# Kernel tuning notes

Hardware: AMD Instinct MI355X
Metric: run time of the kernel (lower is better)

The kernel has to match this reference:

```python
import jax, jax.numpy as jnp
import numpy as np

NUM_HEAD = 8
B, NO, LQ, LC, D = 16, 512, 512, 512, 1024


def setup_inputs() -> dict:
    key = jax.random.key(0)
    ks = jax.random.split(key, 32)
    s = 0.02

    def lin(i, din, dout):
        w = jax.random.normal(ks[i], (din, dout), jnp.float32) * s
        b = jax.random.normal(ks[i + 1], (dout,), jnp.float32) * s
        return w, b

    v = jax.random.normal(ks[20], (B, NO, D), jnp.float32)
    q = jax.random.normal(ks[21], (B, LQ, D), jnp.float32)
    c = jax.random.normal(ks[22], (B, LC, D), jnp.float32)
    # binary float masks; force first position valid so mask.sum > 0
    v_mask = jax.random.randint(ks[23], (B, NO), 0, 2).astype(jnp.float32).at[:, 0].set(1.0)
    q_mask = jax.random.randint(ks[24], (B, LQ), 0, 2).astype(jnp.float32).at[:, 0].set(1.0)
    c_mask = jax.random.randint(ks[25], (B, LC), 0, 2).astype(jnp.float32).at[:, 0].set(1.0)
    v4q_w, v4q_b = lin(0, D, D)
    q4v_w, q4v_b = lin(2, D, D)
    v_lin_w, v_lin_b = lin(4, D, 3 * D)
    q_lin_w, q_lin_b = lin(6, D, 3 * D)
    c_lin_w, c_lin_b = lin(8, D, 3 * D)
    v_out_w, v_out_b = lin(10, D, D)
    q_out_w, q_out_b = lin(12, D, D)
    c_out_w, c_out_b = lin(14, D, D)
    m_v_k = jax.random.normal(ks[16], (1, 1, D), jnp.float32) * s
    m_v_v = jax.random.normal(ks[17], (1, 1, D), jnp.float32) * s
    m_c_k = jax.random.normal(ks[18], (1, 1, D), jnp.float32) * s
    m_c_v = jax.random.normal(ks[19], (1, 1, D), jnp.float32) * s
    return dict(v=v, q=q, c=c, v_mask=v_mask, q_mask=q_mask, c_mask=c_mask,
                v4q_w=v4q_w, v4q_b=v4q_b, q4v_w=q4v_w, q4v_b=q4v_b,
                v_lin_w=v_lin_w, v_lin_b=v_lin_b, q_lin_w=q_lin_w, q_lin_b=q_lin_b,
                c_lin_w=c_lin_w, c_lin_b=c_lin_b,
                m_v_k=m_v_k, m_v_v=m_v_v, m_c_k=m_c_k, m_c_v=m_c_v,
                v_out_w=v_out_w, v_out_b=v_out_b, q_out_w=q_out_w, q_out_b=q_out_b,
                c_out_w=c_out_w, c_out_b=c_out_b)


def _attn(q_in, k_in, v_in, kmask):
    # q_in [B,Sq,D], k_in/v_in [B,Sk,D], kmask [B,Sk]. Vectorized over heads
    # (replaces the per-head Python loop + cat in the torch source).
    Bs, Sq, Dm = q_in.shape
    Sk = k_in.shape[1]
    dh = Dm // NUM_HEAD
    qh = q_in.reshape(Bs, Sq, NUM_HEAD, dh)
    kh = k_in.reshape(Bs, Sk, NUM_HEAD, dh)
    vh = v_in.reshape(Bs, Sk, NUM_HEAD, dh)
    scores = jnp.einsum('bqhd,bkhd->bhqk', qh, kh)
    # torch: masked_fill(-1e9) then divide by sqrt(d_head) -> replicate exactly
    scores = jnp.where(kmask[:, None, None, :] == 0, jnp.float32(-1e9), scores) / (dh ** 0.5)
    w = jax.nn.softmax(scores, axis=-1)
    out = jnp.einsum('bhqk,bkhd->bqhd', w, vh)
    return out.reshape(Bs, Sq, Dm)


def _forward(v, q, c, v_mask, q_mask, c_mask,
             v4q_w, v4q_b, q4v_w, q4v_b,
             v_lin_w, v_lin_b, q_lin_w, q_lin_b, c_lin_w, c_lin_b,
             m_v_k, m_v_v, m_c_k, m_c_v,
             v_out_w, v_out_b, q_out_w, q_out_b, c_out_w, c_out_b):
    Bs = v.shape[0]
    Dm = v_out_w.shape[0]
    relu, sig = jax.nn.relu, jax.nn.sigmoid
    v_mean = (v * v_mask[:, :, None]).sum(1) / v_mask.sum(1, keepdims=True)
    q_mean = (q * q_mask[:, :, None]).sum(1) / q_mask.sum(1, keepdims=True)
    v4q_gate = sig(relu(v_mean) @ v4q_w + v4q_b)[:, None, :]  # gates q's q/k
    q4v_gate = sig(relu(q_mean) @ q4v_w + q4v_b)[:, None, :]  # gates v's q/k
    v_trans = (relu(v) @ v_lin_w + v_lin_b) * v_mask[:, :, None]
    q_trans = (relu(q) @ q_lin_w + q_lin_b) * q_mask[:, :, None]
    c_trans = (relu(c) @ c_lin_w + c_lin_b) * c_mask[:, :, None]
    v_k, v_q, v_v = jnp.split(v_trans, 3, axis=2)
    q_k, q_q, q_v = jnp.split(q_trans, 3, axis=2)
    c_k, c_q, c_v = jnp.split(c_trans, 3, axis=2)
    # memory tokens: k scaled by sqrt(D), v scaled by sqrt(mv)=1 (as in torch)
    mvk = (Dm ** 0.5) * jnp.broadcast_to(m_v_k, (Bs, 1, Dm))
    mvv = jnp.broadcast_to(m_v_v, (Bs, 1, Dm))
    v_k = jnp.concatenate([mvk, v_k], axis=1)
    v_v = jnp.concatenate([mvv, v_v], axis=1)
    v_kmask = jnp.concatenate([jnp.ones((Bs, 1), v_mask.dtype), v_mask], axis=1)
    mck = (Dm ** 0.5) * jnp.broadcast_to(m_c_k, (Bs, 1, Dm))
    mcv = jnp.broadcast_to(m_c_v, (Bs, 1, Dm))
    c_k = jnp.concatenate([mck, c_k], axis=1)
    c_v = jnp.concatenate([mcv, c_v], axis=1)
    c_kmask = jnp.concatenate([jnp.ones((Bs, 1), c_mask.dtype), c_mask], axis=1)
    new_vq = (1.0 + q4v_gate) * v_q
    new_vk = (1.0 + q4v_gate) * v_k
    new_qq = (1.0 + v4q_gate) * q_q
    new_qk = (1.0 + v4q_gate) * q_k
    v_update = _attn(new_vq, new_vk, v_v, v_kmask)
    q_update = _attn(new_qq, new_qk, q_v, q_mask)
    c_update = _attn(c_q, c_k, c_v, c_kmask)
    updated_v = (v + v_update) @ v_out_w + v_out_b
    updated_q = (q + q_update) @ q_out_w + q_out_b
    updated_c = (c + c_update) @ c_out_w + c_out_b
    return updated_v, updated_q, updated_c


def reference(v, q, c, v_mask, q_mask, c_mask,
              v4q_w, v4q_b, q4v_w, q4v_b,
              v_lin_w, v_lin_b, q_lin_w, q_lin_b, c_lin_w, c_lin_b,
              m_v_k, m_v_v, m_c_k, m_c_v,
              v_out_w, v_out_b, q_out_w, q_out_b, c_out_w, c_out_b):
    return _forward(v, q, c, v_mask, q_mask, c_mask,
                    v4q_w, v4q_b, q4v_w, q4v_b,
                    v_lin_w, v_lin_b, q_lin_w, q_lin_b, c_lin_w, c_lin_b,
                    m_v_k, m_v_v, m_c_k, m_c_v,
                    v_out_w, v_out_b, q_out_w, q_out_b, c_out_w, c_out_b)
```

## Files before the change

### kernel.cpp

```cpp
#include <hip/hip_runtime.h>
#include <stdint.h>

typedef __attribute__((ext_vector_type(8))) short s16x8;
typedef __attribute__((ext_vector_type(4))) float f32x4;

#define DM 1024
#define TOK 512
#define LDK 3072

static __device__ __forceinline__ float bf2f(short u) {
  union { unsigned int i; float f; } x;
  x.i = ((unsigned int)(unsigned short)u) << 16;
  return x.f;
}
static __device__ __forceinline__ short f2bf(float f) {
  union { float f; unsigned int i; } x; x.f = f;
  unsigned int r = x.i + 0x7FFFu + ((x.i >> 16) & 1u);
  return (short)(r >> 16);
}
static __device__ __forceinline__ f32x4 fzero4() {
  f32x4 z; z[0]=0.f; z[1]=0.f; z[2]=0.f; z[3]=0.f; return z;
}
static __device__ __forceinline__ s16x8 szero8() {
  s16x8 z; z[0]=0; z[1]=0; z[2]=0; z[3]=0; z[4]=0; z[5]=0; z[6]=0; z[7]=0; return z;
}
static __device__ __forceinline__ void gl_lds16(const short* g, short* s) {
  __builtin_amdgcn_global_load_lds((const __attribute__((address_space(1))) void*)g,
                                   (__attribute__((address_space(3))) void*)s, 16, 0, 0);
}

#define MFMA(a, b, c) __builtin_amdgcn_mfma_f32_16x16x32_bf16(a, b, c, 0, 0, 0)

struct CastArgs { const float* x[3]; short* xb[3]; };
__global__ __launch_bounds__(256) void cast_relu_kernel(CastArgs a) {
  const float* x = a.x[blockIdx.y];
  short* xb = a.xb[blockIdx.y];
  size_t i = ((size_t)blockIdx.x * 256 + threadIdx.x) * 8;
  float4 v0 = *(const float4*)(x + i);
  float4 v1 = *(const float4*)(x + i + 4);
  s16x8 o;
  o[0] = f2bf(fmaxf(v0.x, 0.f)); o[1] = f2bf(fmaxf(v0.y, 0.f));
  o[2] = f2bf(fmaxf(v0.z, 0.f)); o[3] = f2bf(fmaxf(v0.w, 0.f));
  o[4] = f2bf(fmaxf(v1.x, 0.f)); o[5] = f2bf(fmaxf(v1.y, 0.f));
  o[6] = f2bf(fmaxf(v1.z, 0.f)); o[7] = f2bf(fmaxf(v1.w, 0.f));
  *(s16x8*)(xb + i) = o;
}

__global__ __launch_bounds__(256) void mean_kernel(const float* __restrict__ v,
                                                   const float* __restrict__ q,
                                                   const float* __restrict__ vmask,
                                                   const float* __restrict__ qmask,
                                                   float* __restrict__ vmean,
                                                   float* __restrict__ qmean) {
  int d = blockIdx.x * 256 + threadIdx.x;
  int b = blockIdx.y;
  const float* x; const float* mk; float* out;
  if (blockIdx.z == 0) { x = v; mk = vmask; out = vmean; }
  else                 { x = q; mk = qmask; out = qmean; }
  const float* xp = x + ((size_t)b * TOK) * DM + d;
  const float* mp = mk + b * TOK;
  float s = 0.f, ms = 0.f;
#pragma unroll 4
  for (int r = 0; r < TOK; ++r) {
    float m = mp[r];
    ms += m;
    s += xp[(size_t)r * DM] * m;
  }
  out[b * DM + d] = s / ms;
}

struct TransArgs { const float* w[3]; short* wt[3]; };
__global__ void transpose_cast_kernel(TransArgs a, int K, int N) {
  __shared__ float tile[32][33];
  const float* w = a.w[blockIdx.z];
  short* wt = a.wt[blockIdx.z];
  int n0 = blockIdx.x * 32, k0 = blockIdx.y * 32;
  int tx = threadIdx.x, ty = threadIdx.y;
#pragma unroll
  for (int i = 0; i < 32; i += 8)
    tile[ty + i][tx] = w[(size_t)(k0 + ty + i) * N + n0 + tx];
  __syncthreads();
#pragma unroll
  for (int i = 0; i < 32; i += 8)
    wt[(size_t)(n0 + ty + i) * K + k0 + tx] = f2bf(tile[tx][ty + i]);
}

__global__ __launch_bounds__(256) void gate_kernel(const float* __restrict__ vmean,
                                                   const float* __restrict__ qmean,
                                                   const float* __restrict__ v4q_w,
                                                   const float* __restrict__ v4q_b,
                                                   const float* __restrict__ q4v_w,
                                                   const float* __restrict__ q4v_b,
                                                   float* __restrict__ gate_q,
                                                   float* __restrict__ gate_v) {
  int n = blockIdx.x * 256 + threadIdx.x;
  int b = blockIdx.y;
  const float* mean; const float* w; const float* bias; float* out;
  if (blockIdx.z == 0) { mean = vmean; w = v4q_w; bias = v4q_b; out = gate_q; }
  else                 { mean = qmean; w = q4v_w; bias = q4v_b; out = gate_v; }
  float acc = bias[n];
  const float* mp = mean + b * DM;
#pragma unroll 4
  for (int k = 0; k < DM; ++k) {
    float mv = mp[k];
    mv = mv > 0.f ? mv : 0.f;
    acc += mv * w[(size_t)k * DM + n];
  }
  out[b * DM + n] = 1.f + 1.f / (1.f + __expf(-acc));
}

__global__ void kmem_kernel(const float* __restrict__ m_v_k, const float* __restrict__ m_c_k,
                            const float* __restrict__ gate_v,
                            float* __restrict__ kmem_v, float* __restrict__ kmem_c) {
  int d = threadIdx.x;
  int b = blockIdx.x;
  if (b < 16) kmem_v[b * DM + d] = 32.0f * m_v_k[d] * gate_v[b * DM + d];
  else        kmem_c[d] = 32.0f * m_c_k[d];
}

struct CompArgs { const float* mask[3]; int* idx; int* nv; };
__global__ __launch_bounds__(64) void compact_kernel(CompArgs a) {
  int b = blockIdx.x, mod = blockIdx.y;
  const float* mk = a.mask[mod] + b * TOK;
  int* idx = a.idx + (mod * 16 + b) * TOK;
  int l = threadIdx.x;
  int base = 0;
#pragma unroll 1
  for (int ch = 0; ch < 8; ++ch) {
    int pos = ch * 64 + l;
    bool valid = mk[pos] != 0.f;
    unsigned long long bal = __ballot(valid);
    int pre = __popcll(bal & ((1ull << l) - 1ull));
    if (valid) idx[base + pre] = pos;
    base += __popcll(bal);
  }
  if (l == 0) a.nv[mod * 16 + b] = base;
}

struct GemmArgs {
  const short* A[3]; const short* BT[3];
  const float* bias[3]; const float* gate[3];
  short* outB[3]; float* outF[3];
  const int* idx;
  const int* nv;
};
__global__ __launch_bounds__(512) void gemm_kernel(GemmArgs ga, int N, int K) {
  __shared__ short As[128 * 64];
  __shared__ short Bs[128 * 64];
  int z = blockIdx.z;
  const short* A = ga.A[z];
  const short* BT = ga.BT[z];
  const float* bias = ga.bias[z];
  const float* gate = ga.gate[z];
  short* outB = ga.outB[z];
  float* outF = ga.outF[z];

  int bx = blockIdx.x;
  int b = bx >> 2, m0c = (bx & 3) * 128;
  int nvb = TOK;
  const int* idxb = nullptr;
  if (ga.nv != nullptr) {
    nvb = ga.nv[z * 16 + b];
    if (m0c >= nvb) return;
    idxb = ga.idx + (z * 16 + b) * TOK;
  }
  int n0 = blockIdx.y * 128;
  int tid = threadIdx.x;
  int w = tid >> 6, l = tid & 63;
  int wr = w >> 2, wc = w & 3;
  int lg = l >> 4, lo = l & 15;

  int cc = (l & 7) ^ (l >> 3);
  const short* pa[2];
  const short* pb[2];
#pragma unroll
  for (int i = 0; i < 2; ++i) {
    int row = (w * 2 + i) * 8 + (l >> 3);
    int rg = m0c + row;
    if (idxb != nullptr) rg = idxb[(m0c + row < nvb) ? (m0c + row) : 0];
    pa[i] = A + ((size_t)b * TOK + rg) * K + cc * 8;
    pb[i] = BT + (size_t)(n0 + row) * K + cc * 8;
  }

  f32x4 acc[4][2];
#pragma unroll
  for (int i = 0; i < 4; ++i)
#pragma unroll
    for (int j = 0; j < 2; ++j) acc[i][j] = fzero4();

  for (int k0 = 0; k0 < K; k0 += 64) {
#pragma unroll
    for (int i = 0; i < 2; ++i) {
      gl_lds16(pa[i] + k0, As + (w * 2 + i) * 512);
      gl_lds16(pb[i] + k0, Bs + (w * 2 + i) * 512);
    }
    __syncthreads();
#pragma unroll
    for (int ks = 0; ks < 2; ++ks) {
      int lc = ks * 4 + lg;
      s16x8 af[4], bfr[2];
#pragma unroll
      for (int i = 0; i < 4; ++i) {
        int ar = wr * 64 + i * 16 + lo;
        af[i] = *(const s16x8*)(As + ar * 64 + ((lc ^ (ar & 7)) * 8));
      }
#pragma unroll
      for (int j = 0; j < 2; ++j) {
        int br = wc * 32 + j * 16 + lo;
        bfr[j] = *(const s16x8*)(Bs + br * 64 + ((lc ^ (br & 7)) * 8));
      }
#pragma unroll
      for (int i = 0; i < 4; ++i)
#pragma unroll
        for (int j = 0; j < 2; ++j)
          acc[i][j] = MFMA(af[i], bfr[j], acc[i][j]);
    }
    __syncthreads();
  }

#pragma unroll
  for (int i = 0; i < 4; ++i)
#pragma unroll
    for (int j = 0; j < 2; ++j) {
      int rowc = m0c + wr * 64 + i * 16 + (lg << 2);
      int col = n0 + wc * 32 + j * 16 + lo;
      float cs = 1.f;
      if (gate != nullptr && col < 2048) cs = gate[b * DM + (col & 1023)];
      float bv = bias[col];
#pragma unroll
      for (int r = 0; r < 4; ++r) {
        if (rowc + r >= nvb) continue;
        float val = (acc[i][j][r] + bv) * cs;
        size_t orow = (size_t)b * TOK + rowc + r;
        if (outB != nullptr) outB[orow * N + col] = f2bf(val);
        else                 outF[orow * N + col] = val;
      }
    }
}

struct AttnArgs {
  const short* kqv[3];
  const float* kmem[3];
  const float* vmem[3];
  const float* xin[3];
  short* xu[3];
  const int* idx;
  const int* nv;
  int kmem_bstride[3];
};

__global__ __launch_bounds__(512) void attn_kernel(AttnArgs args) {
  __shared__ short Ks[64 * 128];
  __shared__ short Vs[8 * 1032];
  __shared__ short Ps[8 * 1216];
  int bid = blockIdx.x;
  int mod = bid >> 9;
  int r9 = bid & 511;
  int x = r9 & 7, jj = r9 >> 3;
  int p = x * 16 + (jj & 15), qt = jj >> 4;
  int b = p >> 3, h = p & 7;

  int nvb = args.nv[mod * 16 + b];
  if (qt * 128 >= nvb) return;

  const short* kqv  = args.kqv[mod];
  const float* kmem = args.kmem[mod];
  const float* vmem = args.vmem[mod];
  const float* xin  = args.xin[mod];
  short* xu = args.xu[mod];
  const int* idxb = args.idx + (mod * 16 + b) * TOK;
  int kmem_bs = args.kmem_bstride[mod];

  int tid = threadIdx.x;
  int w = tid >> 6, l = tid & 63;
  int lg = l >> 4, lo = l & 15;
  size_t rowbase = (size_t)b * TOK;
  int q0 = qt * 128 + w * 16;
  const float scale = 0.08838834764831845f;
  short* Pw = Ps + w * 1216;
  int nkt = (nvb + 63) >> 6;

  s16x8 ones;
#pragma unroll
  for (int j = 0; j < 8; ++j) ones[j] = (short)0x3F80;

  int qrow = q0 + lo;
  s16x8 qf[4];
#pragma unroll
  for (int c = 0; c < 4; ++c)
    qf[c] = (qrow < nvb)
      ? *(const s16x8*)(kqv + (rowbase + qrow) * LDK + 1024 + h * 128 + c * 32 + lg * 8)
      : szero8();

  float m;
  f32x4 oacc[9];
#pragma unroll
  for (int c = 0; c < 9; ++c) oacc[c] = fzero4();

  if (kmem != nullptr) {
    const float* km = kmem + (size_t)b * kmem_bs + h * 128;
    float part = 0.f;
#pragma unroll
    for (int c = 0; c < 4; ++c)
#pragma unroll
      for (int j = 0; j < 8; ++j)
        part += bf2f(qf[c][j]) * km[c * 32 + lg * 8 + j];
    part += __shfl_xor(part, 16);
    part += __shfl_xor(part, 32);
    float sm = part * scale;
    float sm4[4], w4[4];
#pragma unroll
    for (int r = 0; r < 4; ++r) sm4[r] = __shfl(sm, lg * 4 + r);
    m = fmaxf(fmaxf(sm4[0], sm4[1]), fmaxf(sm4[2], sm4[3]));
#pragma unroll
    for (int r = 0; r < 4; ++r) w4[r] = __expf(sm4[r] - m);
#pragma unroll
    for (int c = 0; c < 8; ++c) {
      float vv = vmem[h * 128 + c * 16 + lo];
#pragma unroll
      for (int r = 0; r < 4; ++r) oacc[c][r] = w4[r] * vv;
    }
#pragma unroll
    for (int r = 0; r < 4; ++r) oacc[8][r] = w4[r];
  } else {
    m = -3.0e38f;
  }

  int c8A = 2 * w, c8B = 2 * w + 1;
  s16x8 vregA = (l < nvb)
    ? *(const s16x8*)(kqv + (rowbase + l) * LDK + 2048 + h * 128 + c8A * 8) : szero8();
  s16x8 vregB = (l < nvb)
    ? *(const s16x8*)(kqv + (rowbase + l) * LDK + 2048 + h * 128 + c8B * 8) : szero8();

#pragma unroll 1
  for (int kt = 0; kt < nkt; ++kt) {
    __syncthreads();
#pragma unroll
    for (int i = 0; i < 2; ++i) {
      int inst = w * 2 + i;
      int row = inst * 4 + lg;
      int csrc = (l & 15) ^ (row & 7);
      gl_lds16(kqv + (rowbase + kt * 64 + row) * LDK + h * 128 + csrc * 8,
               Ks + inst * 512);
    }
    {
      short* baseA = Vs + (l >> 3) * 1032 + c8A * 64 + (l & 7);
      short* baseB = Vs + (l >> 3) * 1032 + c8B * 64 + (l & 7);
#pragma unroll
      for (int j = 0; j < 8; ++j) baseA[j * 8] = vregA[j];
#pragma unroll
      for (int j = 0; j < 8; ++j) baseB[j * 8] = vregB[j];
    }
    __syncthreads();

    if (kt + 1 < nkt) {
      int row2 = (kt + 1) * 64 + l;
      vregA = (row2 < nvb)
        ? *(const s16x8*)(kqv + (rowbase + row2) * LDK + 2048 + h * 128 + c8A * 8) : szero8();
      vregB = (row2 < nvb)
        ? *(const s16x8*)(kqv + (rowbase + row2) * LDK + 2048 + h * 128 + c8B * 8) : szero8();
    }

    f32x4 s4[4];
#pragma unroll
    for (int sub = 0; sub < 4; ++sub) {
      f32x4 acc = fzero4();
      int krow = sub * 16 + lo;
#pragma unroll
      for (int cc = 0; cc < 4; ++cc) {
        s16x8 kf = *(const s16x8*)(Ks + krow * 128 + (((cc * 4 + lg) ^ (lo & 7)) * 8));
        acc = MFMA(qf[cc], kf, acc);
      }
      s4[sub] = acc;
    }

    int pos0 = kt * 64 + lo;
    float a[4][4];
    float pmax = -3.0e38f;
#pragma unroll
    for (int r = 0; r < 4; ++r) {
      a[0][r] = (pos0      < nvb) ? s4[0][r] * scale : -1e9f;
      a[1][r] = (pos0 + 16 < nvb) ? s4[1][r] * scale : -1e9f;
      a[2][r] = (pos0 + 32 < nvb) ? s4[2][r] * scale : -1e9f;
      a[3][r] = (pos0 + 48 < nvb) ? s4[3][r] * scale : -1e9f;
      pmax = fmaxf(pmax, fmaxf(fmaxf(a[0][r], a[1][r]), fmaxf(a[2][r], a[3][r])));
    }
    pmax = fmaxf(pmax, __shfl_xor(pmax, 1));
    pmax = fmaxf(pmax, __shfl_xor(pmax, 2));
    pmax = fmaxf(pmax, __shfl_xor(pmax, 4));
    pmax = fmaxf(pmax, __shfl_xor(pmax, 8));
    if (!__all(pmax - m <= 8.0f)) {
      float nm = fmaxf(m, pmax);
      float f = __expf(m - nm);
#pragma unroll
      for (int c = 0; c < 9; ++c)
#pragma unroll
        for (int r = 0; r < 4; ++r) oacc[c][r] *= f;
      m = nm;
    }

#pragma unroll
    for (int sub = 0; sub < 4; ++sub)
#pragma unroll
      for (int r = 0; r < 4; ++r)
        Pw[(lg * 4 + r) * 76 + sub * 16 + lo] = f2bf(__expf(a[sub][r] - m));

    s16x8 pf0 = *(const s16x8*)(Pw + lo * 76 + lg * 8);
    s16x8 pf1 = *(const s16x8*)(Pw + lo * 76 + 32 + lg * 8);
#pragma unroll
    for (int c = 0; c < 8; ++c) {
      s16x8 vf0 = *(const s16x8*)(Vs + lg * 1032 + (c * 16 + lo) * 8);
      s16x8 vf1 = *(const s16x8*)(Vs + (4 + lg) * 1032 + (c * 16 + lo) * 8);
      oacc[c] = MFMA(pf0, vf0, oacc[c]);
      oacc[c] = MFMA(pf1, vf1, oacc[c]);
    }
    oacc[8] = MFMA(pf0, ones, oacc[8]);
    oacc[8] = MFMA(pf1, ones, oacc[8]);
  }

  int orig[4];
#pragma unroll
  for (int r = 0; r < 4; ++r) {
    int crow = q0 + lg * 4 + r;
    orig[r] = (crow < nvb) ? idxb[crow] : -1;
  }
  float invl[4];
#pragma unroll
  for (int r = 0; r < 4; ++r) invl[r] = 1.f / oacc[8][r];
#pragma unroll
  for (int c = 0; c < 8; ++c)
#pragma unroll
    for (int r = 0; r < 4; ++r) {
      if (orig[r] < 0) continue;
      size_t row = rowbase + orig[r];
      int col = h * 128 + c * 16 + lo;
      float val = oacc[c][r] * invl[r] + xin[row * DM + col];
      xu[row * DM + col] = f2bf(val);
    }
}

struct UniArgs {
  const short* kqv[3]; const float* mask[3]; const float* mem[3];
  const float* xin[3]; short* xu[3]; const int* nv;
};
__global__ __launch_bounds__(1024) void uniform_fill_kernel(UniArgs a) {
  __shared__ float part[8][1024];
  int b = blockIdx.x, mod = blockIdx.y;
  int nvb = a.nv[mod * 16 + b];
  const short* kv = a.kqv[mod];
  int tid = threadIdx.x;
  int g = tid >> 7;
  int dd = tid & 127;

  f32x4 p0 = fzero4(), p1 = fzero4();
#pragma unroll 2
  for (int r = g; r < nvb; r += 8) {
    s16x8 vv = *(const s16x8*)(kv + ((size_t)b * TOK + r) * LDK + 2048 + dd * 8);
#pragma unroll
    for (int j = 0; j < 4; ++j) { p0[j] += bf2f(vv[j]); p1[j] += bf2f(vv[4 + j]); }
  }
  *(f32x4*)&part[g][dd * 8] = p0;
  *(f32x4*)&part[g][dd * 8 + 4] = p1;
  __syncthreads();
  {
    float s = 0.f;
#pragma unroll
    for (int gg = 0; gg < 8; ++gg) s += part[gg][tid];
    float denom = (float)nvb;
    if (a.mem[mod] != nullptr) { s += a.mem[mod][tid]; denom += 1.f; }
    __syncthreads();
    part[0][tid] = s / denom;
  }
  __syncthreads();
  float avg[8];
#pragma unroll
  for (int j = 0; j < 8; ++j) avg[j] = part[0][dd * 8 + j];

  const float* mk = a.mask[mod] + b * TOK;
  const float* x = a.xin[mod];
  short* xu = a.xu[mod];
#pragma unroll 1
  for (int rb = 0; rb < TOK; rb += 8) {
    int r = rb + g;
    if (mk[r] != 0.f) continue;
    size_t base = ((size_t)b * TOK + r) * DM + dd * 8;
    float4 x0 = *(const float4*)(x + base);
    float4 x1 = *(const float4*)(x + base + 4);
    s16x8 o;
    o[0] = f2bf(x0.x + avg[0]); o[1] = f2bf(x0.y + avg[1]);
    o[2] = f2bf(x0.z + avg[2]); o[3] = f2bf(x0.w + avg[3]);
    o[4] = f2bf(x1.x + avg[4]); o[5] = f2bf(x1.y + avg[5]);
    o[6] = f2bf(x1.z + avg[6]); o[7] = f2bf(x1.w + avg[7]);
    *(s16x8*)(xu + base) = o;
  }
}

extern "C" void kernel_launch(void* const* d_in, const int* in_sizes, int n_in,
                              void* d_out, int out_size, void* d_ws, size_t ws_size,
                              hipStream_t stream) {
  const float* v      = (const float*)d_in[0];
  const float* q      = (const float*)d_in[1];
  const float* c      = (const float*)d_in[2];
  const float* v_mask = (const float*)d_in[3];
  const float* q_mask = (const float*)d_in[4];
  const float* c_mask = (const float*)d_in[5];
  const float* v4q_w  = (const float*)d_in[6];
  const float* v4q_b  = (const float*)d_in[7];
  const float* q4v_w  = (const float*)d_in[8];
  const float* q4v_b  = (const float*)d_in[9];
  const float* v_lin_w = (const float*)d_in[10];
  const float* v_lin_b = (const float*)d_in[11];
  const float* q_lin_w = (const float*)d_in[12];
  const float* q_lin_b = (const float*)d_in[13];
  const float* c_lin_w = (const float*)d_in[14];
  const float* c_lin_b = (const float*)d_in[15];
  const float* m_v_k  = (const float*)d_in[16];
  const float* m_v_v  = (const float*)d_in[17];
  const float* m_c_k  = (const float*)d_in[18];
  const float* m_c_v  = (const float*)d_in[19];
  const float* v_out_w = (const float*)d_in[20];
  const float* v_out_b = (const float*)d_in[21];
  const float* q_out_w = (const float*)d_in[22];
  const float* q_out_b = (const float*)d_in[23];
  const float* c_out_w = (const float*)d_in[24];
  const float* c_out_b = (const float*)d_in[25];

  const size_t MB = 1024ull * 1024ull;
  char* ws = (char*)d_ws;
  short* xbf_v = (short*)(ws + 0 * MB);
  short* xbf_q = (short*)(ws + 16 * MB);
  short* xbf_c = (short*)(ws + 32 * MB);
  short* wt_lin_v = (short*)(ws + 48 * MB);
  short* wt_lin_q = (short*)(ws + 54 * MB);
  short* wt_lin_c = (short*)(ws + 60 * MB);
  short* wt_out_v = (short*)(ws + 66 * MB);
  short* wt_out_q = (short*)(ws + 68 * MB);
  short* wt_out_c = (short*)(ws + 70 * MB);
  short* kqv_v = (short*)(ws + 72 * MB);
  short* kqv_q = (short*)(ws + 120 * MB);
  short* kqv_c = (short*)(ws + 168 * MB);
  float* vmean  = (float*)(ws + 216 * MB);
  float* qmean  = vmean + 16 * 1024;
  float* gate_q = qmean + 16 * 1024;
  float* gate_v = gate_q + 16 * 1024;
  float* kmem_v = gate_v + 16 * 1024;
  float* kmem_c = kmem_v + 16 * 1024;
  int* idxbuf = (int*)(ws + 217 * MB);
  int* nvbuf  = (int*)(ws + 218 * MB);

  CastArgs ca;
  ca.x[0] = v; ca.x[1] = q; ca.x[2] = c;
  ca.xb[0] = xbf_v; ca.xb[1] = xbf_q; ca.xb[2] = xbf_c;
  cast_relu_kernel<<<dim3(4096, 3), 256, 0, stream>>>(ca);
  mean_kernel<<<dim3(4, 16, 2), 256, 0, stream>>>(v, q, v_mask, q_mask, vmean, qmean);

  TransArgs tl;
  tl.w[0] = v_lin_w; tl.w[1] = q_lin_w; tl.w[2] = c_lin_w;
  tl.wt[0] = wt_lin_v; tl.wt[1] = wt_lin_q; tl.wt[2] = wt_lin_c;
  transpose_cast_kernel<<<dim3(96, 32, 3), dim3(32, 8), 0, stream>>>(tl, 1024, 3072);
  TransArgs to;
  to.w[0] = v_out_w; to.w[1] = q_out_w; to.w[2] = c_out_w;
  to.wt[0] = wt_out_v; to.wt[1] = wt_out_q; to.wt[2] = wt_out_c;
  transpose_cast_kernel<<<dim3(32, 32, 3), dim3(32, 8), 0, stream>>>(to, 1024, 1024);

  gate_kernel<<<dim3(4, 16, 2), 256, 0, stream>>>(vmean, qmean, v4q_w, v4q_b, q4v_w, q4v_b,
                                                  gate_q, gate_v);
  kmem_kernel<<<17, 1024, 0, stream>>>(m_v_k, m_c_k, gate_v, kmem_v, kmem_c);

  CompArgs cpa;
  cpa.mask[0] = v_mask; cpa.mask[1] = q_mask; cpa.mask[2] = c_mask;
  cpa.idx = idxbuf; cpa.nv = nvbuf;
  compact_kernel<<<dim3(16, 3), 64, 0, stream>>>(cpa);

  GemmArgs gt;
  gt.A[0] = xbf_v; gt.A[1] = xbf_q; gt.A[2] = xbf_c;
  gt.BT[0] = wt_lin_v; gt.BT[1] = wt_lin_q; gt.BT[2] = wt_lin_c;
  gt.bias[0] = v_lin_b; gt.bias[1] = q_lin_b; gt.bias[2] = c_lin_b;
  gt.gate[0] = gate_v; gt.gate[1] = gate_q; gt.gate[2] = nullptr;
  gt.outB[0] = kqv_v; gt.outB[1] = kqv_q; gt.outB[2] = kqv_c;
  gt.outF[0] = nullptr; gt.outF[1] = nullptr; gt.outF[2] = nullptr;
  gt.idx = idxbuf; gt.nv = nvbuf;
  gemm_kernel<<<dim3(64, 24, 3), 512, 0, stream>>>(gt, 3072, 1024);

  AttnArgs aa;
  aa.kqv[0] = kqv_v; aa.kqv[1] = kqv_q; aa.kqv[2] = kqv_c;
  aa.kmem[0] = kmem_v; aa.kmem[1] = nullptr; aa.kmem[2] = kmem_c;
  aa.vmem[0] = m_v_v; aa.vmem[1] = nullptr; aa.vmem[2] = m_c_v;
  aa.xin[0] = v; aa.xin[1] = q; aa.xin[2] = c;
  aa.xu[0] = xbf_v; aa.xu[1] = xbf_q; aa.xu[2] = xbf_c;
  aa.idx = idxbuf; aa.nv = nvbuf;
  aa.kmem_bstride[0] = 1024; aa.kmem_bstride[1] = 0; aa.kmem_bstride[2] = 0;
  attn_kernel<<<1536, 512, 0, stream>>>(aa);

  UniArgs ua;
  ua.kqv[0] = kqv_v; ua.kqv[1] = kqv_q; ua.kqv[2] = kqv_c;
  ua.mask[0] = v_mask; ua.mask[1] = q_mask; ua.mask[2] = c_mask;
  ua.mem[0] = m_v_v; ua.mem[1] = nullptr; ua.mem[2] = m_c_v;
  ua.xin[0] = v; ua.xin[1] = q; ua.xin[2] = c;
  ua.xu[0] = xbf_v; ua.xu[1] = xbf_q; ua.xu[2] = xbf_c;
  ua.nv = nvbuf;
  uniform_fill_kernel<<<dim3(16, 3), 1024, 0, stream>>>(ua);

  float* outp = (float*)d_out;
  GemmArgs go;
  go.A[0] = xbf_v; go.A[1] = xbf_q; go.A[2] = xbf_c;
  go.BT[0] = wt_out_v; go.BT[1] = wt_out_q; go.BT[2] = wt_out_c;
  go.bias[0] = v_out_b; go.bias[1] = q_out_b; go.bias[2] = c_out_b;
  go.gate[0] = nullptr; go.gate[1] = nullptr; go.gate[2] = nullptr;
  go.outB[0] = nullptr; go.outB[1] = nullptr; go.outB[2] = nullptr;
  go.outF[0] = outp; go.outF[1] = outp + 8388608; go.outF[2] = outp + 16777216;
  go.idx = nullptr; go.nv = nullptr;
  gemm_kernel<<<dim3(64, 8, 3), 512, 0, stream>>>(go, 1024, 1024);
}
```

Before: 630.7 us.

## Split fused QKV projection GEMM into per-stream kernels with larger M tiles

Replaces the single batched projection GEMM launch over the three streams with three launches. The v stream keeps the original kernel, while q and c use new kernels with 256-row M tiles (one with 1024 threads, one with 512 threads and a 4x4 MFMA tile per wave). The larger row tiles are meant to improve reuse of the weight tile across compacted rows. The cost is three serialized launches on one stream instead of one, and possibly lower occupancy from the larger blocks.

```diff
diff --git a/kernel.cpp b/kernel.cpp
--- a/kernel.cpp
+++ b/kernel.cpp
@@ -234,6 +234,179 @@
         size_t orow = (size_t)b * TOK + rowc + r;
         if (outB != nullptr) outB[orow * N + col] = f2bf(val);
         else                 outF[orow * N + col] = val;
+      }
+    }
+}
+
+__global__ __launch_bounds__(1024) void gemmB_kernel(const short* __restrict__ A,
+                                                     const short* __restrict__ BT,
+                                                     const float* __restrict__ bias,
+                                                     const float* __restrict__ gate,
+                                                     short* __restrict__ outB,
+                                                     const int* __restrict__ idxm,
+                                                     const int* __restrict__ nvm,
+                                                     int N, int K) {
+  __shared__ short As[256 * 64];
+  __shared__ short Bs[128 * 64];
+  int bx = blockIdx.x;
+  int b = bx >> 1, m0c = (bx & 1) * 256;
+  int nvb = nvm[b];
+  if (m0c >= nvb) return;
+  const int* idxb = idxm + b * TOK;
+  int n0 = blockIdx.y * 128;
+  int tid = threadIdx.x;
+  int w = tid >> 6, l = tid & 63;
+  int wr = w >> 2, wc = w & 3;
+  int lg = l >> 4, lo = l & 15;
+  int cc = (l & 7) ^ (l >> 3);
+
+  const short* pa[2];
+#pragma unroll
+  for (int i = 0; i < 2; ++i) {
+    int row = (w * 2 + i) * 8 + (l >> 3);
+    int rg = idxb[(m0c + row < nvb) ? (m0c + row) : 0];
+    pa[i] = A + ((size_t)b * TOK + rg) * K + cc * 8;
+  }
+  const short* pbp = BT + (size_t)(n0 + w * 8 + (l >> 3)) * K + cc * 8;
+
+  f32x4 acc[4][2];
+#pragma unroll
+  for (int i = 0; i < 4; ++i)
+#pragma unroll
+    for (int j = 0; j < 2; ++j) acc[i][j] = fzero4();
+
+  for (int k0 = 0; k0 < K; k0 += 64) {
+#pragma unroll
+    for (int i = 0; i < 2; ++i)
+      gl_lds16(pa[i] + k0, As + (w * 2 + i) * 512);
+    gl_lds16(pbp + k0, Bs + w * 512);
+    __syncthreads();
+#pragma unroll
+    for (int ks = 0; ks < 2; ++ks) {
+      int lc = ks * 4 + lg;
+      s16x8 af[4], bfr[2];
+#pragma unroll
+      for (int i = 0; i < 4; ++i) {
+        int ar = wr * 64 + i * 16 + lo;
+        af[i] = *(const s16x8*)(As + ar * 64 + ((lc ^ (ar & 7)) * 8));
+      }
+#pragma unroll
+      for (int j = 0; j < 2; ++j) {
+        int br = wc * 32 + j * 16 + lo;
+        bfr[j] = *(const s16x8*)(Bs + br * 64 + ((lc ^ (br & 7)) * 8));
+      }
+#pragma unroll
+      for (int i = 0; i < 4; ++i)
+#pragma unroll
+        for (int j = 0; j < 2; ++j)
+          acc[i][j] = MFMA(af[i], bfr[j], acc[i][j]);
+    }
+    __syncthreads();
+  }
+
+#pragma unroll
+  for (int i = 0; i < 4; ++i)
+#pragma unroll
+    for (int j = 0; j < 2; ++j) {
+      int rowc = m0c + wr * 64 + i * 16 + (lg << 2);
+      int col = n0 + wc * 32 + j * 16 + lo;
+      float cs = 1.f;
+      if (gate != nullptr && col < 2048) cs = gate[b * DM + (col & 1023)];
+      float bv = bias[col];
+#pragma unroll
+      for (int r = 0; r < 4; ++r) {
+        if (rowc + r >= nvb) continue;
+        float val = (acc[i][j][r] + bv) * cs;
+        outB[((size_t)b * TOK + rowc + r) * N + col] = f2bf(val);
+      }
+    }
+}
+
+__global__ __launch_bounds__(512) void gemmC_kernel(const short* __restrict__ A,
+                                                    const short* __restrict__ BT,
+                                                    const float* __restrict__ bias,
+                                                    const float* __restrict__ gate,
+                                                    short* __restrict__ outB,
+                                                    const int* __restrict__ idxm,
+                                                    const int* __restrict__ nvm,
+                                                    int N, int K) {
+  __shared__ short As[256 * 64];
+  __shared__ short Bs[128 * 64];
+  int bx = blockIdx.x;
+  int b = bx >> 1, m0c = (bx & 1) * 256;
+  int nvb = nvm[b];
+  if (m0c >= nvb) return;
+  const int* idxb = idxm + b * TOK;
+  int n0 = blockIdx.y * 128;
+  int tid = threadIdx.x;
+  int w = tid >> 6, l = tid & 63;
+  int wr = w >> 1, wc = w & 1;
+  int lg = l >> 4, lo = l & 15;
+  int cc = (l & 7) ^ (l >> 3);
+
+  const short* pa[4];
+#pragma unroll
+  for (int i = 0; i < 4; ++i) {
+    int row = (w * 4 + i) * 8 + (l >> 3);
+    int rg = idxb[(m0c + row < nvb) ? (m0c + row) : 0];
+    pa[i] = A + ((size_t)b * TOK + rg) * K + cc * 8;
+  }
+  const short* pb[2];
+#pragma unroll
+  for (int i = 0; i < 2; ++i)
+    pb[i] = BT + (size_t)(n0 + (w * 2 + i) * 8 + (l >> 3)) * K + cc * 8;
+
+  f32x4 acc[4][4];
+#pragma unroll
+  for (int i = 0; i < 4; ++i)
+#pragma unroll
+    for (int j = 0; j < 4; ++j) acc[i][j] = fzero4();
+
+  for (int k0 = 0; k0 < K; k0 += 64) {
+#pragma unroll
+    for (int i = 0; i < 4; ++i)
+      gl_lds16(pa[i] + k0, As + (w * 4 + i) * 512);
+#pragma unroll
+    for (int i = 0; i < 2; ++i)
+      gl_lds16(pb[i] + k0, Bs + (w * 2 + i) * 512);
+    __syncthreads();
+#pragma unroll
+    for (int ks = 0; ks < 2; ++ks) {
+      int lc = ks * 4 + lg;
+      s16x8 af[4], bfr[4];
+#pragma unroll
+      for (int i = 0; i < 4; ++i) {
+        int ar = wr * 64 + i * 16 + lo;
+        af[i] = *(const s16x8*)(As + ar * 64 + ((lc ^ (ar & 7)) * 8));
+      }
+#pragma unroll
+      for (int j = 0; j < 4; ++j) {
+        int br = wc * 64 + j * 16 + lo;
+        bfr[j] = *(const s16x8*)(Bs + br * 64 + ((lc ^ (br & 7)) * 8));
+      }
+#pragma unroll
+      for (int i = 0; i < 4; ++i)
+#pragma unroll
+        for (int j = 0; j < 4; ++j)
+          acc[i][j] = MFMA(af[i], bfr[j], acc[i][j]);
+    }
+    __syncthreads();
+  }
+
+#pragma unroll
+  for (int i = 0; i < 4; ++i)
+#pragma unroll
+    for (int j = 0; j < 4; ++j) {
+      int rowc = m0c + wr * 64 + i * 16 + (lg << 2);
+      int col = n0 + wc * 64 + j * 16 + lo;
+      float cs = 1.f;
+      if (gate != nullptr && col < 2048) cs = gate[b * DM + (col & 1023)];
+      float bv = bias[col];
+#pragma unroll
+      for (int r = 0; r < 4; ++r) {
+        if (rowc + r >= nvb) continue;
+        float val = (acc[i][j][r] + bv) * cs;
+        outB[((size_t)b * TOK + rowc + r) * N + col] = f2bf(val);
       }
     }
 }
@@ -572,15 +745,20 @@
   cpa.idx = idxbuf; cpa.nv = nvbuf;
   compact_kernel<<<dim3(16, 3), 64, 0, stream>>>(cpa);
 
-  GemmArgs gt;
-  gt.A[0] = xbf_v; gt.A[1] = xbf_q; gt.A[2] = xbf_c;
-  gt.BT[0] = wt_lin_v; gt.BT[1] = wt_lin_q; gt.BT[2] = wt_lin_c;
-  gt.bias[0] = v_lin_b; gt.bias[1] = q_lin_b; gt.bias[2] = c_lin_b;
-  gt.gate[0] = gate_v; gt.gate[1] = gate_q; gt.gate[2] = nullptr;
-  gt.outB[0] = kqv_v; gt.outB[1] = kqv_q; gt.outB[2] = kqv_c;
-  gt.outF[0] = nullptr; gt.outF[1] = nullptr; gt.outF[2] = nullptr;
-  gt.idx = idxbuf; gt.nv = nvbuf;
-  gemm_kernel<<<dim3(64, 24, 3), 512, 0, stream>>>(gt, 3072, 1024);
+  GemmArgs gA;
+  gA.A[0] = xbf_v; gA.BT[0] = wt_lin_v; gA.bias[0] = v_lin_b; gA.gate[0] = gate_v;
+  gA.outB[0] = kqv_v; gA.outF[0] = nullptr;
+  gA.A[1] = gA.A[2] = nullptr; gA.BT[1] = gA.BT[2] = nullptr;
+  gA.bias[1] = gA.bias[2] = nullptr; gA.gate[1] = gA.gate[2] = nullptr;
+  gA.outB[1] = gA.outB[2] = nullptr; gA.outF[1] = gA.outF[2] = nullptr;
+  gA.idx = idxbuf; gA.nv = nvbuf;
+  gemm_kernel<<<dim3(64, 24, 1), 512, 0, stream>>>(gA, 3072, 1024);
+  gemmB_kernel<<<dim3(32, 24), 1024, 0, stream>>>(xbf_q, wt_lin_q, q_lin_b, gate_q,
+                                                  kqv_q, idxbuf + 16 * TOK, nvbuf + 16,
+                                                  3072, 1024);
+  gemmC_kernel<<<dim3(32, 24), 512, 0, stream>>>(xbf_c, wt_lin_c, c_lin_b, nullptr,
+                                                 kqv_c, idxbuf + 32 * TOK, nvbuf + 32,
+                                                 3072, 1024);
 
   AttnArgs aa;
   aa.kqv[0] = kqv_v; aa.kqv[1] = kqv_q; aa.kqv[2] = kqv_c;
```

Result: slower. 665.8 us (+5.6%).
